# Performance work log

Measured on AMD Instinct MI355X. Metric: run time of the kernel, lower is better.

## Reference

```python
import jax, jax.numpy as jnp
import numpy as np

TOP_K = 2  # config.num_experts_per_tok


def setup_inputs() -> dict:
    key = jax.random.key(0)
    ks = jax.random.split(key, 5)
    B, S, H, I, E = 4, 2048, 512, 1024, 8
    x = jax.random.normal(ks[0], (B, S, H), dtype=jnp.float32)
    gate_w = jax.random.normal(ks[1], (E, H), dtype=jnp.float32) * 0.02  # router weight, init std 0.02
    w1 = jax.random.normal(ks[2], (E, H, I), dtype=jnp.float32) * (1.0 / np.sqrt(H))
    b1 = jnp.zeros((E, I), dtype=jnp.float32)
    w2 = jax.random.normal(ks[3], (E, I, H), dtype=jnp.float32) * (1.0 / np.sqrt(I))
    b2 = jnp.zeros((E, H), dtype=jnp.float32)
    return {"x": x, "gate_w": gate_w, "w1": w1, "b1": b1, "w2": w2, "b2": b2}


def reference(x, gate_w, w1, b1, w2, b2):
    # Eval mode: no router noise, dropout is identity. capacity = T*top_k -> no drops.
    B, S, H = x.shape
    T = B * S
    E = gate_w.shape[0]
    xf = x.reshape(T, H)
    # Router (computed in fp32, as in the original gate)
    router_logits = xf.astype(jnp.float32) @ gate_w.astype(jnp.float32).T  # [T, E]
    router_probs = jax.nn.softmax(router_logits, axis=-1)
    topk_w, topk_i = jax.lax.top_k(router_probs, TOP_K)  # [T, K]
    # norm_topk_prob=True
    topk_w = topk_w / (jnp.sum(topk_w, axis=-1, keepdims=True) + 1e-20)
    topk_w = topk_w / TOP_K
    # Scatter top-k weights into dense per-expert combine weights [T, E]
    combine = jnp.zeros((T, E), dtype=router_probs.dtype)
    combine = combine.at[jnp.arange(T)[:, None], topk_i].add(topk_w)
    # Per-expert MLP: Linear(H,I) -> ReLU -> Linear(I,H), combined with routing weights
    h = jax.nn.relu(jnp.einsum('th,ehi->tei', xf, w1) + b1[None])  # [T, E, I]
    y = jnp.einsum('tei,eih->teh', h, w2) + b2[None]                # [T, E, H]
    routed_out = jnp.einsum('teh,te->th', y, combine).reshape(B, S, H)
    return routed_out, router_logits
```

## Files before the change

### kernel.cpp

```cpp
#include <hip/hip_runtime.h>
#include <hip/hip_bf16.h>

typedef __attribute__((ext_vector_type(8))) short s16x8;
typedef __attribute__((ext_vector_type(4))) float f32x4;

#define T_TOK 8192
#define H_DIM 512
#define I_DIM 1024

static __device__ __forceinline__ unsigned short f2bf(float f){
  unsigned int b = __builtin_bit_cast(unsigned int, f);
  b += 0x7FFFu + ((b >> 16) & 1u);
  return (unsigned short)(b >> 16);
}

__global__ void transpose_cvt(const float* __restrict__ in, unsigned short* __restrict__ out,
                              int R, int C){
  __shared__ unsigned short tile[64][72];
  int e = blockIdx.z;
  const float* src = in + (size_t)e * R * C;
  unsigned short* dst = out + (size_t)e * R * C;
  int r0 = blockIdx.y * 64, c0 = blockIdx.x * 64;
  int tr = threadIdx.x >> 4;
  int tc = (threadIdx.x & 15) * 4;
  #pragma unroll
  for (int i = 0; i < 4; i++){
    int r = tr + i * 16;
    float4 v = *reinterpret_cast<const float4*>(src + (size_t)(r0 + r) * C + c0 + tc);
    tile[tc + 0][r] = f2bf(v.x);
    tile[tc + 1][r] = f2bf(v.y);
    tile[tc + 2][r] = f2bf(v.z);
    tile[tc + 3][r] = f2bf(v.w);
  }
  __syncthreads();
  #pragma unroll
  for (int i = 0; i < 4; i++){
    int cl = tr + i * 16;
    ushort4 o;
    o.x = tile[cl][tc + 0]; o.y = tile[cl][tc + 1];
    o.z = tile[cl][tc + 2]; o.w = tile[cl][tc + 3];
    *reinterpret_cast<ushort4*>(dst + (size_t)(c0 + cl) * R + r0 + tc) = o;
  }
}

__global__ void router_kernel(const float* __restrict__ x, const float* __restrict__ gw,
                              float* __restrict__ logits_out,
                              int* __restrict__ eab, float* __restrict__ wab,
                              unsigned short* __restrict__ xb){
  int wave = threadIdx.x >> 6;
  int lane = threadIdx.x & 63;
  int t = blockIdx.x * 4 + wave;
  const float* xr = x + (size_t)t * H_DIM;
  float xv[8];
  *reinterpret_cast<float4*>(&xv[0]) = *reinterpret_cast<const float4*>(xr + lane * 8);
  *reinterpret_cast<float4*>(&xv[4]) = *reinterpret_cast<const float4*>(xr + lane * 8 + 4);
  s16x8 xo;
  #pragma unroll
  for (int m = 0; m < 8; m++) xo[m] = (short)f2bf(xv[m]);
  *reinterpret_cast<s16x8*>(xb + (size_t)t * H_DIM + lane * 8) = xo;

  float l[8];
  #pragma unroll
  for (int e = 0; e < 8; e++){
    const float* g = gw + e * H_DIM + lane * 8;
    float4 g0 = *reinterpret_cast<const float4*>(g);
    float4 g1 = *reinterpret_cast<const float4*>(g + 4);
    float s = xv[0]*g0.x + xv[1]*g0.y + xv[2]*g0.z + xv[3]*g0.w
            + xv[4]*g1.x + xv[5]*g1.y + xv[6]*g1.z + xv[7]*g1.w;
    #pragma unroll
    for (int o = 32; o >= 1; o >>= 1) s += __shfl_xor(s, o);
    l[e] = s;
  }
  if (lane == 0){
    float4 L0 = make_float4(l[0], l[1], l[2], l[3]);
    float4 L1 = make_float4(l[4], l[5], l[6], l[7]);
    *reinterpret_cast<float4*>(logits_out + (size_t)t * 8)     = L0;
    *reinterpret_cast<float4*>(logits_out + (size_t)t * 8 + 4) = L1;
    float m = l[0];
    #pragma unroll
    for (int e = 1; e < 8; e++) m = fmaxf(m, l[e]);
    float p[8]; float Z = 0.f;
    #pragma unroll
    for (int e = 0; e < 8; e++){ p[e] = expf(l[e] - m); Z += p[e]; }
    int a = 0;
    #pragma unroll
    for (int e = 1; e < 8; e++) if (p[e] > p[a]) a = e;
    int b = (a == 0) ? 1 : 0;
    #pragma unroll
    for (int e = 0; e < 8; e++) if (e != a && p[e] > p[b]) b = e;
    float pa = p[a] / Z, pb = p[b] / Z;
    float inv = 0.5f / (pa + pb + 1e-20f);
    eab[t] = a | (b << 8);
    *reinterpret_cast<float2*>(wab + (size_t)t * 2) = make_float2(pa * inv, pb * inv);
  }
}

__global__ __launch_bounds__(256) void scatter_kernel(
    const int* __restrict__ eab, const float* __restrict__ wab,
    int* __restrict__ cnt, int* __restrict__ tok, float* __restrict__ wgt){
  __shared__ int wcnt[8][8];
  __shared__ int lbase[8][8];
  __shared__ int gbase[8];
  int tid = threadIdx.x;
  int wave = tid >> 6, lane = tid & 63;
  int t = blockIdx.x * 256 + tid;
  int ee = eab[t];
  int ea = ee & 0xff, eb = ee >> 8;
  float2 wv = *reinterpret_cast<const float2*>(wab + (size_t)t * 2);
  unsigned long long mlt = (1ull << lane) - 1ull;
  int rankA = 0, rankB = 0;
  #pragma unroll
  for (int e = 0; e < 8; e++){
    unsigned long long mA = __ballot(ea == e);
    unsigned long long mB = __ballot(eb == e);
    if (ea == e) rankA = __popcll(mA & mlt);
    if (eb == e) rankB = __popcll(mB & mlt);
    if (lane == 0){
      wcnt[wave * 2 + 0][e] = __popcll(mA);
      wcnt[wave * 2 + 1][e] = __popcll(mB);
    }
  }
  __syncthreads();
  if (tid < 8){
    int s = 0;
    #pragma unroll
    for (int w = 0; w < 8; w++){ lbase[w][tid] = s; s += wcnt[w][tid]; }
    gbase[tid] = atomicAdd(&cnt[tid], s);
  }
  __syncthreads();
  int ia = gbase[ea] + lbase[wave * 2 + 0][ea] + rankA;
  tok[ea * T_TOK + ia] = t; wgt[ea * T_TOK + ia] = wv.x;
  int ib = gbase[eb] + lbase[wave * 2 + 1][eb] + rankB;
  tok[eb * T_TOK + ib] = t; wgt[eb * T_TOK + ib] = wv.y;
}

__global__ void build_tiles(const int* __restrict__ cnt, int* __restrict__ off,
                            int* __restrict__ tmap){
  if (threadIdx.x == 0){
    int s = 0;
    for (int e = 0; e < 8; e++){ off[e] = s; s += cnt[e]; }
    int nt = 0;
    for (int e = 0; e < 8; e++)
      for (int b = 0; b < cnt[e]; b += 64)
        tmap[nt++] = (b << 3) | e;
    off[8] = nt;
  }
}

__global__ __launch_bounds__(256) void gemm1_kernel(
    const unsigned short* __restrict__ xb, const unsigned short* __restrict__ w1t,
    const float* __restrict__ b1,
    const int* __restrict__ cnt, const int* __restrict__ off,
    const int* __restrict__ tok, const int* __restrict__ tmap,
    unsigned short* __restrict__ h_buf){
  int nt = off[8];
  int tile = blockIdx.x;
  if (tile >= nt) return;
  int tmv = tmap[tile];
  int e = tmv & 7, base = tmv >> 3;
  int n_e = cnt[e];
  int offe = off[e];
  int n0 = blockIdx.y * 128;

  __shared__ unsigned short As[64 * 72];
  __shared__ unsigned short Bs[128 * 72];

  int tid = threadIdx.x;
  int lane = tid & 63, wid = tid >> 6;
  int cc = (tid & 7) * 8;
  int sr = tid >> 3;

  const unsigned short* a_src[2];
  #pragma unroll
  for (int j = 0; j < 2; j++){
    int gr = base + sr + j * 32; if (gr >= n_e) gr = n_e - 1;
    a_src[j] = xb + (size_t)tok[e * T_TOK + gr] * H_DIM + cc;
  }
  const unsigned short* b_src[4];
  const unsigned short* Bg = w1t + ((size_t)e * I_DIM + n0) * H_DIM;
  #pragma unroll
  for (int j = 0; j < 4; j++)
    b_src[j] = Bg + (size_t)(sr + j * 32) * H_DIM + cc;

  int wm = (wid >> 1) * 32, wn = (wid & 1) * 64;
  int rfrag = lane & 15;
  int koff  = (lane >> 4) * 8;

  f32x4 acc[2][4] = {};

  for (int k0 = 0; k0 < H_DIM; k0 += 64){
    #pragma unroll
    for (int j = 0; j < 2; j++)
      *reinterpret_cast<int4*>(&As[(sr + j * 32) * 72 + cc]) =
          *reinterpret_cast<const int4*>(a_src[j] + k0);
    #pragma unroll
    for (int j = 0; j < 4; j++)
      *reinterpret_cast<int4*>(&Bs[(sr + j * 32) * 72 + cc]) =
          *reinterpret_cast<const int4*>(b_src[j] + k0);
    __syncthreads();
    #pragma unroll
    for (int kk = 0; kk < 2; kk++){
      s16x8 af[2], bfr[4];
      #pragma unroll
      for (int fm = 0; fm < 2; fm++)
        af[fm] = *reinterpret_cast<const s16x8*>(&As[(wm + fm * 16 + rfrag) * 72 + kk * 32 + koff]);
      #pragma unroll
      for (int fn = 0; fn < 4; fn++)
        bfr[fn] = *reinterpret_cast<const s16x8*>(&Bs[(wn + fn * 16 + rfrag) * 72 + kk * 32 + koff]);
      #pragma unroll
      for (int fm = 0; fm < 2; fm++){
        #pragma unroll
        for (int fn = 0; fn < 4; fn++)
          acc[fm][fn] = __builtin_amdgcn_mfma_f32_16x16x32_bf16(af[fm], bfr[fn], acc[fm][fn], 0, 0, 0);
      }
    }
    __syncthreads();
  }

  int rbase = wm + (lane >> 4) * 4;
  #pragma unroll
  for (int fm = 0; fm < 2; fm++){
    #pragma unroll
    for (int j = 0; j < 4; j++){
      int gr = base + rbase + fm * 16 + j;
      if (gr < n_e){
        #pragma unroll
        for (int fn = 0; fn < 4; fn++){
          int col = n0 + wn + fn * 16 + rfrag;
          float h = acc[fm][fn][j] + b1[e * I_DIM + col];
          h_buf[(size_t)(offe + gr) * I_DIM + col] = f2bf(fmaxf(h, 0.f));
        }
      }
    }
  }
}

__global__ __launch_bounds__(256) void gemm2_kernel(
    const unsigned short* __restrict__ h_buf, const unsigned short* __restrict__ w2t,
    const float* __restrict__ b2,
    const int* __restrict__ cnt, const int* __restrict__ off,
    const int* __restrict__ tok, const float* __restrict__ wgt,
    const int* __restrict__ tmap,
    float* __restrict__ out){
  int nt = off[8];
  int tile = blockIdx.x;
  if (tile >= nt) return;
  int tmv = tmap[tile];
  int e = tmv & 7, base = tmv >> 3;
  int n_e = cnt[e];
  int offe = off[e];
  int n0 = blockIdx.y * 128;

  __shared__ unsigned short As[64 * 72];
  __shared__ unsigned short Bs[128 * 72];
  __shared__ int tok_s[64];
  __shared__ float wgt_s[64];

  int tid = threadIdx.x;
  if (tid < 64){
    int gr = base + tid;
    int gi = (gr < n_e) ? gr : (n_e - 1);
    tok_s[tid] = tok[e * T_TOK + gi];
    wgt_s[tid] = wgt[e * T_TOK + gi];
  }

  int lane = tid & 63, wid = tid >> 6;
  int cc = (tid & 7) * 8;
  int sr = tid >> 3;

  const unsigned short* a_src[2];
  #pragma unroll
  for (int j = 0; j < 2; j++){
    int gr = base + sr + j * 32; if (gr >= n_e) gr = n_e - 1;
    a_src[j] = h_buf + (size_t)(offe + gr) * I_DIM + cc;
  }
  const unsigned short* b_src[4];
  const unsigned short* Bg = w2t + ((size_t)e * H_DIM + n0) * I_DIM;
  #pragma unroll
  for (int j = 0; j < 4; j++)
    b_src[j] = Bg + (size_t)(sr + j * 32) * I_DIM + cc;

  int wm = (wid >> 1) * 32, wn = (wid & 1) * 64;
  int rfrag = lane & 15;
  int koff  = (lane >> 4) * 8;

  f32x4 acc[2][4] = {};

  for (int k0 = 0; k0 < I_DIM; k0 += 64){
    #pragma unroll
    for (int j = 0; j < 2; j++)
      *reinterpret_cast<int4*>(&As[(sr + j * 32) * 72 + cc]) =
          *reinterpret_cast<const int4*>(a_src[j] + k0);
    #pragma unroll
    for (int j = 0; j < 4; j++)
      *reinterpret_cast<int4*>(&Bs[(sr + j * 32) * 72 + cc]) =
          *reinterpret_cast<const int4*>(b_src[j] + k0);
    __syncthreads();
    #pragma unroll
    for (int kk = 0; kk < 2; kk++){
      s16x8 af[2], bfr[4];
      #pragma unroll
      for (int fm = 0; fm < 2; fm++)
        af[fm] = *reinterpret_cast<const s16x8*>(&As[(wm + fm * 16 + rfrag) * 72 + kk * 32 + koff]);
      #pragma unroll
      for (int fn = 0; fn < 4; fn++)
        bfr[fn] = *reinterpret_cast<const s16x8*>(&Bs[(wn + fn * 16 + rfrag) * 72 + kk * 32 + koff]);
      #pragma unroll
      for (int fm = 0; fm < 2; fm++){
        #pragma unroll
        for (int fn = 0; fn < 4; fn++)
          acc[fm][fn] = __builtin_amdgcn_mfma_f32_16x16x32_bf16(af[fm], bfr[fn], acc[fm][fn], 0, 0, 0);
      }
    }
    __syncthreads();
  }

  int rbase = wm + (lane >> 4) * 4;
  #pragma unroll
  for (int fm = 0; fm < 2; fm++){
    #pragma unroll
    for (int j = 0; j < 4; j++){
      int row_l = rbase + fm * 16 + j;
      int gr = base + row_l;
      if (gr < n_e){
        int t = tok_s[row_l];
        float wv = wgt_s[row_l];
        #pragma unroll
        for (int fn = 0; fn < 4; fn++){
          int col = n0 + wn + fn * 16 + rfrag;
          float y = acc[fm][fn][j] + b2[e * H_DIM + col];
          atomicAdd(out + (size_t)t * H_DIM + col, wv * y);
        }
      }
    }
  }
}

extern "C" void kernel_launch(void* const* d_in, const int* in_sizes, int n_in,
                              void* d_out, int out_size, void* d_ws, size_t ws_size,
                              hipStream_t stream){
  const float* x  = (const float*)d_in[0];
  const float* gw = (const float*)d_in[1];
  const float* w1 = (const float*)d_in[2];
  const float* b1 = (const float*)d_in[3];
  const float* w2 = (const float*)d_in[4];
  const float* b2 = (const float*)d_in[5];
  float* out = (float*)d_out;

  char* ws = (char*)d_ws;
  int*   cnt  = (int*)(ws);
  int*   off  = (int*)(ws + 64);
  int*   tmap = (int*)(ws + 128);
  int*   tok  = (int*)(ws + 4096);
  float* wgt  = (float*)(ws + 4096 + 262144);
  unsigned short* xb    = (unsigned short*)(ws + 528384);
  unsigned short* w1t   = (unsigned short*)(ws + 8916992);
  unsigned short* w2t   = (unsigned short*)(ws + 17305600);
  unsigned short* h_buf = (unsigned short*)(ws + 25694208);
  int*   eab = (int*)(ws + 59248640);
  float* wab = (float*)(ws + 59281408);

  hipMemsetAsync(d_out, 0, (size_t)out_size * 4, stream);
  hipMemsetAsync(cnt, 0, 64, stream);

  transpose_cvt<<<dim3(16, 8, 8), 256, 0, stream>>>(w1, w1t, 512, 1024);
  transpose_cvt<<<dim3(8, 16, 8), 256, 0, stream>>>(w2, w2t, 1024, 512);

  float* logits_out = out + (size_t)T_TOK * H_DIM;
  router_kernel<<<2048, 256, 0, stream>>>(x, gw, logits_out, eab, wab, xb);
  scatter_kernel<<<32, 256, 0, stream>>>(eab, wab, cnt, tok, wgt);
  build_tiles<<<1, 64, 0, stream>>>(cnt, off, tmap);

  gemm1_kernel<<<dim3(264, 8), 256, 0, stream>>>(xb, w1t, b1, cnt, off, tok, tmap, h_buf);
  gemm2_kernel<<<dim3(264, 4), 256, 0, stream>>>(h_buf, w2t, b2, cnt, off, tok, wgt, tmap, out);
}
```

Baseline: 237.1 us.

## Double-buffer GEMM tiles via direct global-to-LDS loads with XOR swizzle

Both expert GEMM kernels now copy A and B tiles straight from global memory into LDS with global_load_lds, skipping the round trip through registers. The tiles are double-buffered so the load of the next K step overlaps the MFMA work on the current one. The padded LDS layout is replaced by an XOR-swizzled 64-column layout to avoid bank conflicts. This doubles LDS use per block, which may lower occupancy, and it relies on the wait and barrier placement to keep the async loads correct.

```diff
diff --git a/kernel.cpp b/kernel.cpp
--- a/kernel.cpp
+++ b/kernel.cpp
@@ -12,6 +12,13 @@
   unsigned int b = __builtin_bit_cast(unsigned int, f);
   b += 0x7FFFu + ((b >> 16) & 1u);
   return (unsigned short)(b >> 16);
+}
+
+static __device__ __forceinline__ void g2l16(const void* g, void* l){
+  __builtin_amdgcn_global_load_lds(
+      (__attribute__((address_space(1))) void*)(unsigned long long)g,
+      (__attribute__((address_space(3))) void*)(unsigned int)(unsigned long long)l,
+      16, 0, 0);
 }
 
 __global__ void transpose_cvt(const float* __restrict__ in, unsigned short* __restrict__ out,
@@ -162,51 +169,64 @@
   int offe = off[e];
   int n0 = blockIdx.y * 128;
 
-  __shared__ unsigned short As[64 * 72];
-  __shared__ unsigned short Bs[128 * 72];
+  __shared__ unsigned short As[2][64 * 64];
+  __shared__ unsigned short Bs[2][128 * 64];
 
   int tid = threadIdx.x;
-  int lane = tid & 63, wid = tid >> 6;
-  int cc = (tid & 7) * 8;
-  int sr = tid >> 3;
+  int lane = tid & 63, w = tid >> 6;
+  int gc = (lane & 7) ^ (lane >> 3);
 
   const unsigned short* a_src[2];
   #pragma unroll
   for (int j = 0; j < 2; j++){
-    int gr = base + sr + j * 32; if (gr >= n_e) gr = n_e - 1;
-    a_src[j] = xb + (size_t)tok[e * T_TOK + gr] * H_DIM + cc;
+    int r = w * 16 + j * 8 + (lane >> 3);
+    int gr = base + r; if (gr >= n_e) gr = n_e - 1;
+    a_src[j] = xb + (size_t)tok[e * T_TOK + gr] * H_DIM + gc * 8;
   }
   const unsigned short* b_src[4];
   const unsigned short* Bg = w1t + ((size_t)e * I_DIM + n0) * H_DIM;
   #pragma unroll
   for (int j = 0; j < 4; j++)
-    b_src[j] = Bg + (size_t)(sr + j * 32) * H_DIM + cc;
-
-  int wm = (wid >> 1) * 32, wn = (wid & 1) * 64;
+    b_src[j] = Bg + (size_t)(w * 32 + j * 8 + (lane >> 3)) * H_DIM + gc * 8;
+
+  int wm = (w >> 1) * 32, wn = (w & 1) * 64;
   int rfrag = lane & 15;
-  int koff  = (lane >> 4) * 8;
+  int g4 = lane >> 4;
 
   f32x4 acc[2][4] = {};
 
-  for (int k0 = 0; k0 < H_DIM; k0 += 64){
-    #pragma unroll
-    for (int j = 0; j < 2; j++)
-      *reinterpret_cast<int4*>(&As[(sr + j * 32) * 72 + cc]) =
-          *reinterpret_cast<const int4*>(a_src[j] + k0);
-    #pragma unroll
-    for (int j = 0; j < 4; j++)
-      *reinterpret_cast<int4*>(&Bs[(sr + j * 32) * 72 + cc]) =
-          *reinterpret_cast<const int4*>(b_src[j] + k0);
-    __syncthreads();
+  #pragma unroll
+  for (int j = 0; j < 2; j++) g2l16(a_src[j], &As[0][(w * 16 + j * 8) * 64]);
+  #pragma unroll
+  for (int j = 0; j < 4; j++) g2l16(b_src[j], &Bs[0][(w * 32 + j * 8) * 64]);
+  __syncthreads();
+
+  int cur = 0;
+  const int NSTEP = H_DIM / 64;
+  for (int t = 0; t < NSTEP; t++){
+    if (t + 1 < NSTEP){
+      int k1 = (t + 1) * 64;
+      #pragma unroll
+      for (int j = 0; j < 2; j++) g2l16(a_src[j] + k1, &As[cur ^ 1][(w * 16 + j * 8) * 64]);
+      #pragma unroll
+      for (int j = 0; j < 4; j++) g2l16(b_src[j] + k1, &Bs[cur ^ 1][(w * 32 + j * 8) * 64]);
+    }
+    const unsigned short* Ac = &As[cur][0];
+    const unsigned short* Bc = &Bs[cur][0];
     #pragma unroll
     for (int kk = 0; kk < 2; kk++){
+      int g = kk * 4 + g4;
       s16x8 af[2], bfr[4];
       #pragma unroll
-      for (int fm = 0; fm < 2; fm++)
-        af[fm] = *reinterpret_cast<const s16x8*>(&As[(wm + fm * 16 + rfrag) * 72 + kk * 32 + koff]);
-      #pragma unroll
-      for (int fn = 0; fn < 4; fn++)
-        bfr[fn] = *reinterpret_cast<const s16x8*>(&Bs[(wn + fn * 16 + rfrag) * 72 + kk * 32 + koff]);
+      for (int fm = 0; fm < 2; fm++){
+        int r = wm + fm * 16 + rfrag;
+        af[fm] = *reinterpret_cast<const s16x8*>(&Ac[r * 64 + ((g ^ (r & 7)) * 8)]);
+      }
+      #pragma unroll
+      for (int fn = 0; fn < 4; fn++){
+        int r = wn + fn * 16 + rfrag;
+        bfr[fn] = *reinterpret_cast<const s16x8*>(&Bc[r * 64 + ((g ^ (r & 7)) * 8)]);
+      }
       #pragma unroll
       for (int fm = 0; fm < 2; fm++){
         #pragma unroll
@@ -215,6 +235,7 @@
       }
     }
     __syncthreads();
+    cur ^= 1;
   }
 
   int rbase = wm + (lane >> 4) * 4;
@@ -251,8 +272,8 @@
   int offe = off[e];
   int n0 = blockIdx.y * 128;
 
-  __shared__ unsigned short As[64 * 72];
-  __shared__ unsigned short Bs[128 * 72];
+  __shared__ unsigned short As[2][64 * 64];
+  __shared__ unsigned short Bs[2][128 * 64];
   __shared__ int tok_s[64];
   __shared__ float wgt_s[64];
 
@@ -264,47 +285,60 @@
     wgt_s[tid] = wgt[e * T_TOK + gi];
   }
 
-  int lane = tid & 63, wid = tid >> 6;
-  int cc = (tid & 7) * 8;
-  int sr = tid >> 3;
+  int lane = tid & 63, w = tid >> 6;
+  int gc = (lane & 7) ^ (lane >> 3);
 
   const unsigned short* a_src[2];
   #pragma unroll
   for (int j = 0; j < 2; j++){
-    int gr = base + sr + j * 32; if (gr >= n_e) gr = n_e - 1;
-    a_src[j] = h_buf + (size_t)(offe + gr) * I_DIM + cc;
+    int r = w * 16 + j * 8 + (lane >> 3);
+    int gr = base + r; if (gr >= n_e) gr = n_e - 1;
+    a_src[j] = h_buf + (size_t)(offe + gr) * I_DIM + gc * 8;
   }
   const unsigned short* b_src[4];
   const unsigned short* Bg = w2t + ((size_t)e * H_DIM + n0) * I_DIM;
   #pragma unroll
   for (int j = 0; j < 4; j++)
-    b_src[j] = Bg + (size_t)(sr + j * 32) * I_DIM + cc;
-
-  int wm = (wid >> 1) * 32, wn = (wid & 1) * 64;
+    b_src[j] = Bg + (size_t)(w * 32 + j * 8 + (lane >> 3)) * I_DIM + gc * 8;
+
+  int wm = (w >> 1) * 32, wn = (w & 1) * 64;
   int rfrag = lane & 15;
-  int koff  = (lane >> 4) * 8;
+  int g4 = lane >> 4;
 
   f32x4 acc[2][4] = {};
 
-  for (int k0 = 0; k0 < I_DIM; k0 += 64){
-    #pragma unroll
-    for (int j = 0; j < 2; j++)
-      *reinterpret_cast<int4*>(&As[(sr + j * 32) * 72 + cc]) =
-          *reinterpret_cast<const int4*>(a_src[j] + k0);
-    #pragma unroll
-    for (int j = 0; j < 4; j++)
-      *reinterpret_cast<int4*>(&Bs[(sr + j * 32) * 72 + cc]) =
-          *reinterpret_cast<const int4*>(b_src[j] + k0);
-    __syncthreads();
+  #pragma unroll
+  for (int j = 0; j < 2; j++) g2l16(a_src[j], &As[0][(w * 16 + j * 8) * 64]);
+  #pragma unroll
+  for (int j = 0; j < 4; j++) g2l16(b_src[j], &Bs[0][(w * 32 + j * 8) * 64]);
+  __syncthreads();
+
+  int cur = 0;
+  const int NSTEP = I_DIM / 64;
+  for (int t = 0; t < NSTEP; t++){
+    if (t + 1 < NSTEP){
+      int k1 = (t + 1) * 64;
+      #pragma unroll
+      for (int j = 0; j < 2; j++) g2l16(a_src[j] + k1, &As[cur ^ 1][(w * 16 + j * 8) * 64]);
+      #pragma unroll
+      for (int j = 0; j < 4; j++) g2l16(b_src[j] + k1, &Bs[cur ^ 1][(w * 32 + j * 8) * 64]);
+    }
+    const unsigned short* Ac = &As[cur][0];
+    const unsigned short* Bc = &Bs[cur][0];
     #pragma unroll
     for (int kk = 0; kk < 2; kk++){
+      int g = kk * 4 + g4;
       s16x8 af[2], bfr[4];
       #pragma unroll
-      for (int fm = 0; fm < 2; fm++)
-        af[fm] = *reinterpret_cast<const s16x8*>(&As[(wm + fm * 16 + rfrag) * 72 + kk * 32 + koff]);
-      #pragma unroll
-      for (int fn = 0; fn < 4; fn++)
-        bfr[fn] = *reinterpret_cast<const s16x8*>(&Bs[(wn + fn * 16 + rfrag) * 72 + kk * 32 + koff]);
+      for (int fm = 0; fm < 2; fm++){
+        int r = wm + fm * 16 + rfrag;
+        af[fm] = *reinterpret_cast<const s16x8*>(&Ac[r * 64 + ((g ^ (r & 7)) * 8)]);
+      }
+      #pragma unroll
+      for (int fn = 0; fn < 4; fn++){
+        int r = wn + fn * 16 + rfrag;
+        bfr[fn] = *reinterpret_cast<const s16x8*>(&Bc[r * 64 + ((g ^ (r & 7)) * 8)]);
+      }
       #pragma unroll
       for (int fm = 0; fm < 2; fm++){
         #pragma unroll
@@ -313,6 +347,7 @@
       }
     }
     __syncthreads();
+    cur ^= 1;
   }
 
   int rbase = wm + (lane >> 4) * 4;
```

After: 214.5 us. 9.5% less time.
